# Optimization experiments

Measured on AMD Instinct MI355X. Metric: run time of the kernel, lower is better.

The kernel has to match this reference:

```python
import jax, jax.numpy as jnp
import numpy as np

DIM = 384
HEADS = 12
POS_DIM = (DIM // 4) // 4  # DynamicPosBias: pos_dim = (dim//4)//4 = 24
B_WIN = 64
GH = GW = GD = 8
N_TOK = GH * GW * GD  # 512
NG = 8  # num windows sharing one mask


def _ln(x, g, b):
    m = jnp.mean(x, axis=-1, keepdims=True)
    v = jnp.var(x, axis=-1, keepdims=True)
    return (x - m) / jnp.sqrt(v + 1e-5) * g + b


def setup_inputs() -> dict:
    key = jax.random.key(0)
    ks = jax.random.split(key, 8)
    s = 0.02
    inp = {
        "x": jax.random.normal(ks[0], (B_WIN, N_TOK, DIM), jnp.float32),
        "H": GH, "W": GW, "D": GD,
        "mask": jnp.zeros((NG, N_TOK, N_TOK), jnp.float32),
        "qkv_w": jax.random.normal(ks[1], (DIM, 3 * DIM), jnp.float32) * s,
        "qkv_b": jnp.zeros((3 * DIM,), jnp.float32),
        "proj_w": jax.random.normal(ks[2], (DIM, DIM), jnp.float32) * s,
        "proj_b": jnp.zeros((DIM,), jnp.float32),
        "pos_proj_w": jax.random.normal(ks[3], (3, POS_DIM), jnp.float32) * s,
        "pos_proj_b": jnp.zeros((POS_DIM,), jnp.float32),
        "ln1_g": jnp.ones((POS_DIM,), jnp.float32), "ln1_b": jnp.zeros((POS_DIM,), jnp.float32),
        "pos1_w": jax.random.normal(ks[4], (POS_DIM, POS_DIM), jnp.float32) * s,
        "pos1_b": jnp.zeros((POS_DIM,), jnp.float32),
        "ln2_g": jnp.ones((POS_DIM,), jnp.float32), "ln2_b": jnp.zeros((POS_DIM,), jnp.float32),
        "pos2_w": jax.random.normal(ks[5], (POS_DIM, POS_DIM), jnp.float32) * s,
        "pos2_b": jnp.zeros((POS_DIM,), jnp.float32),
        "ln3_g": jnp.ones((POS_DIM,), jnp.float32), "ln3_b": jnp.zeros((POS_DIM,), jnp.float32),
        "pos3_w": jax.random.normal(ks[6], (POS_DIM, HEADS), jnp.float32) * s,
        "pos3_b": jnp.zeros((HEADS,), jnp.float32),
    }
    return inp


def reference(x, H, W, D, mask, qkv_w, qkv_b, proj_w, proj_b,
              pos_proj_w, pos_proj_b, ln1_g, ln1_b, pos1_w, pos1_b,
              ln2_g, ln2_b, pos2_w, pos2_b, ln3_g, ln3_b, pos3_w, pos3_b):
    B_, N, C = x.shape
    h = HEADS
    d = C // h
    scale = d ** (-0.5)

    qkv = (x @ qkv_w + qkv_b).reshape(B_, N, 3, h, d).transpose(2, 0, 3, 1, 4)
    q, k, v = qkv[0] * scale, qkv[1], qkv[2]  # each (B_, h, N, d)

    attn = jnp.einsum('bhnd,bhmd->bhnm', q, k)  # (B_, h, N, N)

    # dynamic relative position bias
    rh = jnp.arange(1 - H, H)
    rw = jnp.arange(1 - W, W)
    rd = jnp.arange(1 - D, D)
    biases = jnp.stack(jnp.meshgrid(rh, rw, rd, indexing='ij'))
    biases = biases.reshape(3, -1).T.astype(jnp.float32)  # (L, 3), L=(2H-1)(2W-1)(2D-1)

    coords = jnp.stack(jnp.meshgrid(jnp.arange(H), jnp.arange(W), jnp.arange(D), indexing='ij'))
    coords = coords.reshape(3, -1)  # (3, N)
    rel = (coords[:, :, None] - coords[:, None, :]).transpose(1, 2, 0)  # (N, N, 3)
    rel = rel + jnp.array([H - 1, W - 1, D - 1])
    rel = rel * jnp.array([(2 * W - 1) * (2 * D - 1), 2 * D - 1, 1])
    rpi = rel.sum(-1)  # (N, N) int index into L

    pos = biases @ pos_proj_w + pos_proj_b  # (L, pos_dim)
    pos = jax.nn.relu(_ln(pos, ln1_g, ln1_b)) @ pos1_w + pos1_b
    pos = jax.nn.relu(_ln(pos, ln2_g, ln2_b)) @ pos2_w + pos2_b
    pos = jax.nn.relu(_ln(pos, ln3_g, ln3_b)) @ pos3_w + pos3_b  # (L, h)

    rel_bias = pos[rpi]  # (N, N, h)
    attn = attn + rel_bias.transpose(2, 0, 1)[None]  # (B_, h, N, N)

    nG = mask.shape[0]
    attn = attn.reshape(B_ // nG, nG, h, N, N) + mask[None, :, None]
    attn = jax.nn.softmax(attn.reshape(B_, h, N, N), axis=-1)

    out = jnp.einsum('bhnm,bhmd->bhnd', attn, v)  # (B_, h, N, d)
    out = out.transpose(0, 2, 1, 3).reshape(B_, N, C)
    return out @ proj_w + proj_b
```

## Files before the change

### kernel.cpp

```cpp
#include <hip/hip_runtime.h>


typedef __bf16 bf16;
typedef __bf16 bf16x4 __attribute__((ext_vector_type(4)));
typedef __bf16 bf16x8 __attribute__((ext_vector_type(8)));
typedef float  f32x4  __attribute__((ext_vector_type(4)));
typedef unsigned int u32;
typedef u32 u32x4v __attribute__((ext_vector_type(4)));

#define DIMC   384
#define HEADS  12
#define HD     32
#define NTOK   512
#define NWIN   64
#define LTAB   3375
#define LPAD   3392
#define PD     24
#define LOG2E  1.4426950408889634f
#define QPRE   (0.17677669529663687f * LOG2E)

#define SZ_WQT  884736ll
#define SZ_WPT  294912ll
#define SZ_POST 81408ll
#define SZ_FLAG 256ll
#define SZ_B2   6291456ll
#define SZ_MT   4194304ll
#define SZ_QKV  25165824ll
#define WS_SMALL 102236160ull
#define WS_BIG   112410368ull

#define NB_XC   12288
#define NB_WQT  1728
#define NB_WPT  576
#define NB_MSK  256
#define NB_POS  14
#define NB_PREP (NB_XC + NB_WQT + NB_WPT + NB_MSK + NB_POS)

#define NB_ATTN (HEADS * NWIN * 4)

__device__ inline u32 cvtpk(float lo, float hi) {
    u32 r;
    asm("v_cvt_pk_bf16_f32 %0, %1, %2" : "=v"(r) : "v"(lo), "v"(hi));
    return r;
}
__device__ inline void plswap32(u32& a, u32& b) {
    asm("v_permlane32_swap_b32 %0, %1" : "+v"(a), "+v"(b));
}
__device__ inline void plswap16(u32& a, u32& b) {
    asm("v_permlane16_swap_b32 %0, %1" : "+v"(a), "+v"(b));
}
__device__ inline float ex2(float x) {
#if __has_builtin(__builtin_amdgcn_exp2f)
    return __builtin_amdgcn_exp2f(x);
#else
    float r; asm("v_exp_f32 %0, %1" : "=v"(r) : "v"(x)); return r;
#endif
}
__device__ inline void gload_lds16(const void* g, void* l) {
    __builtin_amdgcn_global_load_lds(
        (const __attribute__((address_space(1))) void*)g,
        (__attribute__((address_space(3))) void*)l, 16, 0, 0);
}

__device__ inline void ln_relu24(const float* x, const float* __restrict__ g,
                                 const float* __restrict__ b, float* y)
{
    float mean = 0.f;
#pragma unroll
    for (int j = 0; j < PD; j++) mean += x[j];
    mean *= (1.f / PD);
    float var = 0.f;
#pragma unroll
    for (int j = 0; j < PD; j++) { float d = x[j] - mean; var += d * d; }
    var *= (1.f / PD);
    float inv = rsqrtf(var + 1e-5f);
#pragma unroll
    for (int j = 0; j < PD; j++) {
        float t = (x[j] - mean) * inv * g[j] + b[j];
        y[j] = t > 0.f ? t : 0.f;
    }
}

__global__ __launch_bounds__(256) void prep_kernel(
    const float* __restrict__ x,
    const float* __restrict__ qkv_w, const float* __restrict__ proj_w,
    const float* __restrict__ mask,
    const float* __restrict__ pw,  const float* __restrict__ pb,
    const float* __restrict__ g1,  const float* __restrict__ b1,
    const float* __restrict__ w1,  const float* __restrict__ bb1,
    const float* __restrict__ g2,  const float* __restrict__ b2,
    const float* __restrict__ w2,  const float* __restrict__ bb2,
    const float* __restrict__ g3,  const float* __restrict__ b3,
    const float* __restrict__ w3,  const float* __restrict__ bb3,
    bf16* __restrict__ xb, bf16* __restrict__ wqT, bf16* __restrict__ wpT,
    int* __restrict__ flag, bf16* __restrict__ posTg)
{
    const int tid = threadIdx.x;
    int bx = blockIdx.x;

    if (bx < NB_XC) {
        const int i = bx * 256 + tid;
        const f32x4 v = *(const f32x4*)(x + (size_t)i * 4);
        bf16x4 o;
#pragma unroll
        for (int j = 0; j < 4; j++) o[j] = (bf16)v[j];
        *(bf16x4*)(xb + (size_t)i * 4) = o;
        return;
    }
    bx -= NB_XC;
    if (bx < NB_WQT) {
        const int idx = bx * 256 + tid;
        const int n = idx / 384, k = idx - n * 384;
        wqT[idx] = (bf16)qkv_w[(size_t)k * 1152 + n];
        return;
    }
    bx -= NB_WQT;
    if (bx < NB_WPT) {
        const int idx = bx * 256 + tid;
        const int n = idx / 384, k = idx - n * 384;
        wpT[idx] = (bf16)proj_w[(size_t)k * 384 + n];
        return;
    }
    bx -= NB_WPT;
    if (bx < NB_MSK) {
        const int i = bx * 256 + tid;
        const float* p = mask + (size_t)i * 32;
        float s = 0.f;
#pragma unroll
        for (int j = 0; j < 32; j++) s += fabsf(p[j]);
        if (!(s == 0.f)) atomicOr(flag, 1);
        return;
    }
    bx -= NB_MSK;
    {
        const int l = bx * 256 + tid;
        if (l >= LTAB) return;
        const int ih = l / 225, iw = (l / 15) % 15, id = l % 15;
        const float c0 = (float)(ih - 7), c1 = (float)(iw - 7), c2 = (float)(id - 7);
        float xx[PD], y[PD];
#pragma unroll
        for (int j = 0; j < PD; j++)
            xx[j] = c0 * pw[j] + c1 * pw[PD + j] + c2 * pw[2 * PD + j] + pb[j];
        ln_relu24(xx, g1, b1, y);
#pragma unroll
        for (int j = 0; j < PD; j++) {
            float a = bb1[j];
#pragma unroll
            for (int i = 0; i < PD; i++) a += y[i] * w1[i * PD + j];
            xx[j] = a;
        }
        ln_relu24(xx, g2, b2, y);
#pragma unroll
        for (int j = 0; j < PD; j++) {
            float a = bb2[j];
#pragma unroll
            for (int i = 0; i < PD; i++) a += y[i] * w2[i * PD + j];
            xx[j] = a;
        }
        ln_relu24(xx, g3, b3, y);
#pragma unroll
        for (int hh = 0; hh < HEADS; hh++) {
            float a = bb3[hh];
#pragma unroll
            for (int i = 0; i < PD; i++) a += y[i] * w3[i * HEADS + hh];
            posTg[hh * LPAD + l] = (bf16)(a * LOG2E);
        }
    }
}

__global__ __launch_bounds__(256) void bias2_build_kernel(
    const bf16* __restrict__ posTg, bf16* __restrict__ bias2)
{
    int idx = blockIdx.x * 256 + threadIdx.x;
    int h = idx >> 18;
    int q = (idx >> 9) & 511;
    int m = idx & 511;
    int dh = (q >> 6) - (m >> 6) + 7;
    int dw = ((q >> 3) & 7) - ((m >> 3) & 7) + 7;
    int dd = (q & 7) - (m & 7) + 7;
    bias2[idx] = posTg[h * LPAD + dh * 225 + dw * 15 + dd];
}

__global__ __launch_bounds__(256) void vt_inplace_kernel(bf16* __restrict__ V)
{
    __shared__ __align__(16) bf16 tile[32 * 520];
    bf16* base = V + (size_t)blockIdx.x * (NTOK * HD);
    const int tid = threadIdx.x;
    const int nq = tid >> 2;
    const int c4 = tid & 3;
    const int d0 = c4 * 8;
#pragma unroll
    for (int it = 0; it < 8; it++) {
        const int n = nq + it * 64;
        bf16x8 v = *(const bf16x8*)(base + n * HD + d0);
#pragma unroll
        for (int j = 0; j < 8; j++) {
            const int jj = (j + (c4 << 1)) & 7;
            tile[(d0 + jj) * 520 + n] = v[jj];
        }
    }
    __syncthreads();
#pragma unroll
    for (int it = 0; it < 8; it++) {
        const int o = it * 2048 + tid * 8;
        const int d = o >> 9, n = o & 511;
        bf16x8 w = *(const bf16x8*)(tile + d * 520 + n);
        *(bf16x8*)(base + d * NTOK + n) = w;
    }
}

template <int MODE>
__global__ __launch_bounds__(256) void gemm_bt(
    const bf16* __restrict__ A, const bf16* __restrict__ Bt,
    const float* __restrict__ bias,
    bf16* __restrict__ O0, bf16* __restrict__ O1, bf16* __restrict__ O2,
    float* __restrict__ Of, int K, int N)
{
    __shared__ __align__(16) bf16 lA[128 * 64];
    __shared__ __align__(16) bf16 lB[128 * 64];
    const int row0 = blockIdx.x * 128;
    const int col0 = blockIdx.y * 128;
    const int tid  = threadIdx.x;
    const int lane = tid & 63;
    const int wave = tid >> 6;
    const int r0   = (wave >> 1) * 64;
    const int c0   = (wave & 1) * 64;
    const int lrow = lane & 15;
    const int lch  = lane >> 4;

    f32x4 acc[4][4];
    const f32x4 zero4 = {0.f, 0.f, 0.f, 0.f};
#pragma unroll
    for (int i = 0; i < 4; i++)
#pragma unroll
        for (int j = 0; j < 4; j++) acc[i][j] = zero4;

    for (int kt = 0; kt < K; kt += 64) {
        __syncthreads();
#pragma unroll
        for (int it = 0; it < 4; it++) {
            const int c  = tid + it * 256;
            const int rr = c >> 3;
            const int cc = (c & 7) * 8;
            bf16* la = lA + (size_t)(it * 256 + wave * 64) * 8;
            bf16* lb = lB + (size_t)(it * 256 + wave * 64) * 8;
            gload_lds16(A  + (size_t)(row0 + rr) * K + kt + cc, la);
            gload_lds16(Bt + (size_t)(col0 + rr) * K + kt + cc, lb);
        }
        __syncthreads();
#pragma unroll
        for (int kk = 0; kk < 64; kk += 32) {
            bf16x8 af[4], bfr[4];
#pragma unroll
            for (int i = 0; i < 4; i++)
                af[i] = *(const bf16x8*)(lA + (r0 + i * 16 + lrow) * 64 + kk + lch * 8);
#pragma unroll
            for (int j = 0; j < 4; j++)
                bfr[j] = *(const bf16x8*)(lB + (c0 + j * 16 + lrow) * 64 + kk + lch * 8);
#pragma unroll
            for (int i = 0; i < 4; i++)
#pragma unroll
                for (int j = 0; j < 4; j++)
                    acc[i][j] = __builtin_amdgcn_mfma_f32_16x16x32_bf16(af[i], bfr[j], acc[i][j], 0, 0, 0);
        }
    }

#pragma unroll
    for (int i = 0; i < 4; i++) {
#pragma unroll
        for (int j = 0; j < 4; j++) {
#pragma unroll
            for (int r = 0; r < 4; r++) {
                const int mrow = row0 + r0 + i * 16 + lch * 4 + r;
                const int ncol = col0 + c0 + j * 16 + lrow;
                const float v = acc[i][j][r] + bias[ncol];
                if (MODE == 0) {
                    const int t    = ncol >= 768 ? 2 : (ncol >= 384 ? 1 : 0);
                    const int rem2 = ncol - t * 384;
                    const int hh   = rem2 >> 5;
                    const int dd   = rem2 & 31;
                    const int bwin = mrow >> 9;
                    const int n    = mrow & 511;
                    bf16* dst = (t == 0) ? O0 : ((t == 1) ? O1 : O2);
                    const float vv = (t == 0) ? v * QPRE : v;
                    dst[(size_t)((bwin * HEADS + hh) * NTOK + n) * HD + dd] = (bf16)vv;
                } else {
                    Of[(size_t)mrow * N + ncol] = v;
                }
            }
        }
    }
}

template <int BIG>
__global__ __launch_bounds__(256, 4) void attn_kernel(
    const bf16* __restrict__ Qg, const bf16* __restrict__ Kg,
    const bf16* __restrict__ Vtg, const bf16* __restrict__ posTg,
    const float* __restrict__ maskg, const bf16* __restrict__ bias2,
    const int* __restrict__ mflag, bf16* __restrict__ Og)
{
    __shared__ __align__(16) bf16 lPos[BIG ? 16 : LPAD];

    const int idx = (blockIdx.x & 7) * (NB_ATTN / 8) + (blockIdx.x >> 3);
    const int h   = idx >> 8;
    const int rem = idx & 255;
    const int b   = rem >> 2;
    const int qt  = rem & 3;
    const int g   = b & 7;
    const int tid = threadIdx.x;
    const int lane = tid & 63;
    const int wave = tid >> 6;
    const int lrow = lane & 15;
    const int lch  = lane >> 4;
    const int msk  = *mflag;

    const bf16* Qp  = Qg  + (size_t)(b * HEADS + h) * NTOK * HD;
    const bf16* Kp  = Kg  + (size_t)(b * HEADS + h) * NTOK * HD;
    const bf16* Vtp = Vtg + (size_t)(b * HEADS + h) * NTOK * HD;
    const float* Mp = maskg + (size_t)g * NTOK * NTOK;
    const bf16* B2p = bias2 + (size_t)h * NTOK * NTOK;

    if (!BIG) {
        const uint4* src = (const uint4*)(posTg + h * LPAD);
        for (int i = tid; i < LPAD * 2 / 16; i += 256)
            ((uint4*)lPos)[i] = src[i];
        __syncthreads();
    }

    const int qbase = qt * 128 + wave * 32;

    bf16x8 qf[2];
#pragma unroll
    for (int t = 0; t < 2; t++)
        qf[t] = *(const bf16x8*)(Qp + (size_t)(qbase + t * 16 + lrow) * HD + lch * 8);

    int qc0[2] = {0, 0}, qc1[2] = {0, 0}, qc2[2] = {0, 0};
    if (!BIG) {
#pragma unroll
        for (int t = 0; t < 2; t++) {
            const int q = qbase + t * 16 + lrow;
            qc0[t] = q >> 6; qc1[t] = (q >> 3) & 7; qc2[t] = q & 7;
        }
    }

    float m_i[2] = {-1e30f, -1e30f};
    float l_i[2] = {0.f, 0.f};
    f32x4 oacc[2][2];
    const f32x4 zero4 = {0.f, 0.f, 0.f, 0.f};
    oacc[0][0] = zero4; oacc[0][1] = zero4;
    oacc[1][0] = zero4; oacc[1][1] = zero4;

    for (int kt = 0; kt < 4; kt++) {
        bf16x8 apc[2][4];
        float alr[2];

#pragma unroll
        for (int t = 0; t < 2; t++) {
            const int qrow = qbase + t * 16 + lrow;
            f32x4 sf[8];

            bf16x4 bld[8];
            if (BIG) {
                const bf16* brow = B2p + (size_t)qrow * NTOK + kt * 128 + lch * 4;
#pragma unroll
                for (int ct = 0; ct < 8; ct++)
                    bld[ct] = *(const bf16x4*)(brow + ct * 16);
            }

#pragma unroll
            for (int ct = 0; ct < 8; ct++) {
                bf16x8 kf = *(const bf16x8*)(Kp + (size_t)(kt * 128 + ct * 16 + lrow) * HD + lch * 8);
                sf[ct] = __builtin_amdgcn_mfma_f32_16x16x32_bf16(kf, qf[t], zero4, 0, 0, 0);
            }

            if (BIG) {
#pragma unroll
                for (int ct = 0; ct < 8; ct++)
#pragma unroll
                    for (int r = 0; r < 4; r++)
                        sf[ct][r] += (float)bld[ct][r];
            } else {
#pragma unroll
                for (int ct = 0; ct < 8; ct++) {
#pragma unroll
                    for (int r = 0; r < 4; r++) {
                        const int k = kt * 128 + ct * 16 + lch * 4 + r;
                        const int rpi = (qc0[t] - (k >> 6) + 7) * 225
                                      + (qc1[t] - ((k >> 3) & 7) + 7) * 15
                                      + (qc2[t] - (k & 7) + 7);
                        sf[ct][r] += (float)lPos[rpi];
                    }
                }
            }
            if (msk) {
                const float* mrow = Mp + (size_t)qrow * NTOK + kt * 128 + lch * 4;
#pragma unroll
                for (int ct = 0; ct < 8; ct++) {
                    f32x4 mv = *(const f32x4*)(mrow + ct * 16);
#pragma unroll
                    for (int r = 0; r < 4; r++)
                        sf[ct][r] = fmaf(mv[r], LOG2E, sf[ct][r]);
                }
            }

            float px[8];
#pragma unroll
            for (int ct = 0; ct < 8; ct++)
                px[ct] = fmaxf(fmaxf(sf[ct][0], sf[ct][1]), fmaxf(sf[ct][2], sf[ct][3]));
            float mx = fmaxf(fmaxf(fmaxf(px[0], px[1]), fmaxf(px[2], px[3])),
                             fmaxf(fmaxf(px[4], px[5]), fmaxf(px[6], px[7])));
            mx = fmaxf(mx, __shfl_xor(mx, 16));
            mx = fmaxf(mx, __shfl_xor(mx, 32));
            const float mnew = fmaxf(m_i[t], mx);
            const float al   = ex2(m_i[t] - mnew);
            m_i[t] = mnew;
            alr[t] = al;

            float s0 = 0.f, s1 = 0.f;
#pragma unroll
            for (int ct = 0; ct < 8; ct++) {
#pragma unroll
                for (int r = 0; r < 4; r++)
                    sf[ct][r] = ex2(sf[ct][r] - mnew);
                s0 += sf[ct][0] + sf[ct][1];
                s1 += sf[ct][2] + sf[ct][3];
            }
            float ls = s0 + s1;
            ls += __shfl_xor(ls, 16);
            ls += __shfl_xor(ls, 32);
            l_i[t] = l_i[t] * al + ls;

#pragma unroll
            for (int c2 = 0; c2 < 4; c2++) {
                u32 a01 = cvtpk(sf[2 * c2][0],     sf[2 * c2][1]);
                u32 a23 = cvtpk(sf[2 * c2][2],     sf[2 * c2][3]);
                u32 b01 = cvtpk(sf[2 * c2 + 1][0], sf[2 * c2 + 1][1]);
                u32 b23 = cvtpk(sf[2 * c2 + 1][2], sf[2 * c2 + 1][3]);
                plswap32(a01, b01); plswap16(a01, b01);
                plswap32(a23, b23); plswap16(a23, b23);
                u32x4v w; w[0] = a01; w[1] = a23; w[2] = b01; w[3] = b23;
                apc[t][c2] = __builtin_bit_cast(bf16x8, w);
            }
        }

#pragma unroll
        for (int t = 0; t < 2; t++) {
#pragma unroll
            for (int r = 0; r < 4; r++) {
                const float a = __shfl(alr[t], lch * 4 + r);
                oacc[t][0][r] *= a;
                oacc[t][1][r] *= a;
            }
        }

#pragma unroll
        for (int c2 = 0; c2 < 4; c2++) {
            const int mofs = kt * 128 + c2 * 32;
            bf16x8 bv0 = *(const bf16x8*)(Vtp + (size_t)lrow * NTOK + mofs + lch * 8);
            bf16x8 bv1 = *(const bf16x8*)(Vtp + (size_t)(16 + lrow) * NTOK + mofs + lch * 8);
#pragma unroll
            for (int t = 0; t < 2; t++) {
                oacc[t][0] = __builtin_amdgcn_mfma_f32_16x16x32_bf16(apc[t][c2], bv0, oacc[t][0], 0, 0, 0);
                oacc[t][1] = __builtin_amdgcn_mfma_f32_16x16x32_bf16(apc[t][c2], bv1, oacc[t][1], 0, 0, 0);
            }
        }
    }

#pragma unroll
    for (int t = 0; t < 2; t++) {
#pragma unroll
        for (int r = 0; r < 4; r++) {
            const float lv  = __shfl(l_i[t], lch * 4 + r);
            const float inv = 1.f / fmaxf(lv, 1e-20f);
            const int n = qbase + t * 16 + lch * 4 + r;
            bf16* orow = Og + (size_t)(b * NTOK + n) * DIMC + h * HD;
            orow[lrow]      = (bf16)(oacc[t][0][r] * inv);
            orow[16 + lrow] = (bf16)(oacc[t][1][r] * inv);
        }
    }
}

extern "C" void kernel_launch(void* const* d_in, const int* in_sizes, int n_in,
                              void* d_out, int out_size, void* d_ws, size_t ws_size,
                              hipStream_t stream)
{
    if (ws_size < WS_SMALL) return;
    const bool BIG = (ws_size >= WS_BIG);

    const float* x      = (const float*)d_in[0];
    const float* maskp  = (const float*)d_in[4];
    const float* qkv_w  = (const float*)d_in[5];
    const float* qkv_b  = (const float*)d_in[6];
    const float* proj_w = (const float*)d_in[7];
    const float* proj_b = (const float*)d_in[8];

    char* ws = (char*)d_ws;
    size_t off = 0;
    bf16* wsWqT  = (bf16*)(ws + off); off += SZ_WQT;
    bf16* wsWpT  = (bf16*)(ws + off); off += SZ_WPT;
    bf16* wsPosT = (bf16*)(ws + off); off += SZ_POST;
    int*  wsFlag = (int*)(ws + off);  off += SZ_FLAG;
    bf16* wsB2 = nullptr;
    if (BIG) {
        wsB2 = (bf16*)(ws + off); off += SZ_B2;
        off += SZ_MT;
    } else {
        off = 1572864;
    }
    bf16* wsQ    = (bf16*)(ws + off); off += SZ_QKV;
    bf16* wsK    = (bf16*)(ws + off); off += SZ_QKV;
    bf16* wsV    = (bf16*)(ws + off); off += SZ_QKV;
    bf16* wsAttn = (bf16*)(ws + off);
    bf16* wsXb   = wsAttn;

    hipMemsetAsync(wsFlag, 0, 4, stream);

    prep_kernel<<<NB_PREP, 256, 0, stream>>>(
        x, qkv_w, proj_w, maskp,
        (const float*)d_in[9],  (const float*)d_in[10], (const float*)d_in[11],
        (const float*)d_in[12], (const float*)d_in[13], (const float*)d_in[14],
        (const float*)d_in[15], (const float*)d_in[16], (const float*)d_in[17],
        (const float*)d_in[18], (const float*)d_in[19], (const float*)d_in[20],
        (const float*)d_in[21], (const float*)d_in[22],
        wsXb, wsWqT, wsWpT, wsFlag, wsPosT);

    if (BIG)
        bias2_build_kernel<<<(HEADS * NTOK * NTOK) / 256, 256, 0, stream>>>(wsPosT, wsB2);

    gemm_bt<0><<<dim3(256, 9), 256, 0, stream>>>(wsXb, wsWqT, qkv_b, wsQ, wsK, wsV,
                                                 nullptr, 384, 1152);

    vt_inplace_kernel<<<NWIN * HEADS, 256, 0, stream>>>(wsV);

    if (BIG)
        attn_kernel<1><<<NB_ATTN, 256, 0, stream>>>(
            wsQ, wsK, wsV, wsPosT, maskp, wsB2, wsFlag, wsAttn);
    else
        attn_kernel<0><<<NB_ATTN, 256, 0, stream>>>(
            wsQ, wsK, wsV, wsPosT, maskp, wsB2, wsFlag, wsAttn);

    gemm_bt<1><<<dim3(256, 3), 256, 0, stream>>>(wsAttn, wsWpT, proj_b,
                                                 nullptr, nullptr, nullptr,
                                                 (float*)d_out, 384, 384);
}
```

Measured before the change: 455.5 us.

## Stage V tile in LDS and skip online-softmax rescale when max barely moves

Each block now copies its head's transposed V (32x512 bf16) into padded shared memory up front, using direct global-to-LDS loads, and reads V fragments from LDS instead of global memory in the PV MFMA loop. The online softmax also keeps the old running max when no row in the wavefront grows by more than 8 (in log2 units), which skips the exp and the shuffle-based rescale of the accumulators. This adds about 33KB of LDS per block, which may lower occupancy under launch_bounds(256,4). The lazy-rescale threshold lets exponentials reach up to 2^8 before the max is updated, a small accuracy tradeoff.

```diff
diff --git a/kernel.cpp b/kernel.cpp
--- a/kernel.cpp
+++ b/kernel.cpp
@@ -18,6 +18,7 @@
 #define PD     24
 #define LOG2E  1.4426950408889634f
 #define QPRE   (0.17677669529663687f * LOG2E)
+#define VSTR   520
 
 #define SZ_WQT  884736ll
 #define SZ_WPT  294912ll
@@ -299,6 +300,7 @@
     const float* __restrict__ maskg, const bf16* __restrict__ bias2,
     const int* __restrict__ mflag, bf16* __restrict__ Og)
 {
+    __shared__ __align__(16) bf16 lVt[32 * VSTR];
     __shared__ __align__(16) bf16 lPos[BIG ? 16 : LPAD];
 
     const int idx = (blockIdx.x & 7) * (NB_ATTN / 8) + (blockIdx.x >> 3);
@@ -320,12 +322,20 @@
     const float* Mp = maskg + (size_t)g * NTOK * NTOK;
     const bf16* B2p = bias2 + (size_t)h * NTOK * NTOK;
 
+    {
+        const int d0 = wave * 8;
+#pragma unroll
+        for (int rr = 0; rr < 8; rr++) {
+            const int d = d0 + rr;
+            gload_lds16(Vtp + (size_t)d * NTOK + lane * 8, lVt + (size_t)d * VSTR);
+        }
+    }
     if (!BIG) {
         const uint4* src = (const uint4*)(posTg + h * LPAD);
         for (int i = tid; i < LPAD * 2 / 16; i += 256)
             ((uint4*)lPos)[i] = src[i];
-        __syncthreads();
-    }
+    }
+    __syncthreads();
 
     const int qbase = qt * 128 + wave * 32;
 
@@ -353,6 +363,7 @@
     for (int kt = 0; kt < 4; kt++) {
         bf16x8 apc[2][4];
         float alr[2];
+        bool doresc[2];
 
 #pragma unroll
         for (int t = 0; t < 2; t++) {
@@ -411,24 +422,30 @@
                              fmaxf(fmaxf(px[4], px[5]), fmaxf(px[6], px[7])));
             mx = fmaxf(mx, __shfl_xor(mx, 16));
             mx = fmaxf(mx, __shfl_xor(mx, 32));
-            const float mnew = fmaxf(m_i[t], mx);
-            const float al   = ex2(m_i[t] - mnew);
-            m_i[t] = mnew;
-            alr[t] = al;
+
+            if (__all(mx <= m_i[t] + 8.f)) {
+                alr[t] = 1.f;
+                doresc[t] = false;
+            } else {
+                const float mnew = fmaxf(m_i[t], mx);
+                alr[t] = ex2(m_i[t] - mnew);
+                m_i[t] = mnew;
+                doresc[t] = true;
+            }
 
             float s0 = 0.f, s1 = 0.f;
 #pragma unroll
             for (int ct = 0; ct < 8; ct++) {
 #pragma unroll
                 for (int r = 0; r < 4; r++)
-                    sf[ct][r] = ex2(sf[ct][r] - mnew);
+                    sf[ct][r] = ex2(sf[ct][r] - m_i[t]);
                 s0 += sf[ct][0] + sf[ct][1];
                 s1 += sf[ct][2] + sf[ct][3];
             }
             float ls = s0 + s1;
             ls += __shfl_xor(ls, 16);
             ls += __shfl_xor(ls, 32);
-            l_i[t] = l_i[t] * al + ls;
+            l_i[t] = l_i[t] * alr[t] + ls;
 
 #pragma unroll
             for (int c2 = 0; c2 < 4; c2++) {
@@ -445,19 +462,21 @@
 
 #pragma unroll
         for (int t = 0; t < 2; t++) {
-#pragma unroll
-            for (int r = 0; r < 4; r++) {
-                const float a = __shfl(alr[t], lch * 4 + r);
-                oacc[t][0][r] *= a;
-                oacc[t][1][r] *= a;
+            if (doresc[t]) {
+#pragma unroll
+                for (int r = 0; r < 4; r++) {
+                    const float a = __shfl(alr[t], lch * 4 + r);
+                    oacc[t][0][r] *= a;
+                    oacc[t][1][r] *= a;
+                }
             }
         }
 
 #pragma unroll
         for (int c2 = 0; c2 < 4; c2++) {
             const int mofs = kt * 128 + c2 * 32;
-            bf16x8 bv0 = *(const bf16x8*)(Vtp + (size_t)lrow * NTOK + mofs + lch * 8);
-            bf16x8 bv1 = *(const bf16x8*)(Vtp + (size_t)(16 + lrow) * NTOK + mofs + lch * 8);
+            bf16x8 bv0 = *(const bf16x8*)(lVt + (size_t)lrow * VSTR + mofs + lch * 8);
+            bf16x8 bv1 = *(const bf16x8*)(lVt + (size_t)(16 + lrow) * VSTR + mofs + lch * 8);
 #pragma unroll
             for (int t = 0; t < 2; t++) {
                 oacc[t][0] = __builtin_amdgcn_mfma_f32_16x16x32_bf16(apc[t][c2], bv0, oacc[t][0], 0, 0, 0);
```

After: 417.9 us. 1.09x faster.
